# Kernel tuning notes

Measured on AMD Instinct MI355X. Metric: run time of the kernel, lower is better.

Reference implementation:

```python
import jax, jax.numpy as jnp
import numpy as np

TEXT_DIM = 768
IMAGE_DIM = 1024
HIDDEN = 2048
FF = 128
HEADS = 8
HEAD_DIM = HIDDEN // HEADS  # 256


def setup_inputs() -> dict:
    key = jax.random.key(0)
    ks = jax.random.split(key, 16)
    def lin(k, fan_in, fan_out):
        bound = 1.0 / np.sqrt(fan_in)
        kw, kb = jax.random.split(k)
        W = jax.random.uniform(kw, (fan_in, fan_out), jnp.float32, -bound, bound)
        b = jax.random.uniform(kb, (fan_out,), jnp.float32, -bound, bound)
        return W, b
    text = jax.random.normal(ks[0], (16, 512, TEXT_DIM), jnp.float32)
    image = jax.random.normal(ks[1], (16, 576, IMAGE_DIM), jnp.float32)
    wq, bq = lin(ks[2], TEXT_DIM, HIDDEN)
    wk, bk = lin(ks[3], IMAGE_DIM, HIDDEN)
    wv, bv = lin(ks[4], IMAGE_DIM, HIDDEN)
    wr, br = lin(ks[5], HIDDEN, TEXT_DIM)
    w1, b1 = lin(ks[6], TEXT_DIM, FF)
    w2, b2 = lin(ks[7], FF, TEXT_DIM)
    gamma = jnp.ones((TEXT_DIM,), jnp.float32)
    beta = jnp.zeros((TEXT_DIM,), jnp.float32)
    return {"text": text, "image": image,
            "wq": wq, "bq": bq, "wk": wk, "bk": bk, "wv": wv, "bv": bv,
            "wr": wr, "br": br, "w1": w1, "b1": b1, "w2": w2, "b2": b2,
            "gamma": gamma, "beta": beta}


def reference(text, image, wq, bq, wk, bk, wv, bv, wr, br, w1, b1, w2, b2, gamma, beta):
    # Dropout is identity (eval mode).
    bs, lt, _ = text.shape
    li = image.shape[1]
    Q = (text @ wq + bq).reshape(bs, lt, HEADS, HEAD_DIM)
    K = (image @ wk + bk).reshape(bs, li, HEADS, HEAD_DIM)
    V = (image @ wv + bv).reshape(bs, li, HEADS, HEAD_DIM)
    scale = jnp.sqrt(jnp.float32(HEAD_DIM))
    scores = jnp.einsum('bqhd,bkhd->bhqk', Q, K) / scale  # [B,H,Lt,Li]
    attn = jax.nn.softmax(scores, axis=-1)
    x = jnp.einsum('bhqk,bkhd->bqhd', attn, V).reshape(bs, lt, HIDDEN)
    out = x @ wr + br  # [B,Lt,text_dim]
    ff = jax.nn.relu(out @ w1 + b1) @ w2 + b2
    out = out + ff
    # LayerNorm over last dim (eps=1e-5, torch default)
    mu = jnp.mean(out, axis=-1, keepdims=True)
    var = jnp.mean(jnp.square(out - mu), axis=-1, keepdims=True)
    return (out - mu) / jnp.sqrt(var + 1e-5) * gamma + beta
```

## Files before the change

kernel.cpp:

```cpp
#include <hip/hip_runtime.h>
#include <stdint.h>
#include <stddef.h>

typedef __attribute__((ext_vector_type(8))) short bf16x8;
typedef __attribute__((ext_vector_type(4))) float f32x4;

typedef __attribute__((address_space(1))) unsigned int uint_g;
typedef __attribute__((address_space(3))) unsigned int uint_l;

#define DEV static __device__ __forceinline__

DEV unsigned short f2bf(float f) {
  unsigned int u = __float_as_uint(f);
  u += 0x7FFFu + ((u >> 16) & 1u);
  return (unsigned short)(u >> 16);
}

DEV void gl_lds16(const unsigned short* g, unsigned short* l) {
  __builtin_amdgcn_global_load_lds((const uint_g*)g, (uint_l*)l, 16, 0, 0);
}

__global__ __launch_bounds__(256) void k_f32_to_bf16(const float* __restrict__ in,
                                                     unsigned short* __restrict__ out, int n4) {
  int i = blockIdx.x * 256 + threadIdx.x;
  if (i >= n4) return;
  const float4 v = ((const float4*)in)[i];
  ushort4 o;
  o.x = f2bf(v.x); o.y = f2bf(v.y); o.z = f2bf(v.z); o.w = f2bf(v.w);
  ((ushort4*)out)[i] = o;
}

__global__ __launch_bounds__(256) void k_transpose_to_bf16(const float* __restrict__ in,
                                                           unsigned short* __restrict__ out,
                                                           int R, int C) {
  __shared__ unsigned short tile[32][33];
  const int c0 = blockIdx.x << 5, r0 = blockIdx.y << 5;
  const int tx = threadIdx.x & 31, ty = threadIdx.x >> 5;
  #pragma unroll
  for (int i = 0; i < 32; i += 8)
    tile[ty + i][tx] = f2bf(in[(size_t)(r0 + ty + i) * C + c0 + tx]);
  __syncthreads();
  #pragma unroll
  for (int i = 0; i < 32; i += 8)
    out[(size_t)(c0 + ty + i) * R + r0 + tx] = tile[tx][ty + i];
}

enum { EPI_BIAS = 0, EPI_VT = 3, EPI_DUAL = 4, EPI_RELU = 5, EPI_RES = 6 };

template <int BM, int BN, int EPI>
__global__ __launch_bounds__(256)
void k_gemm(const unsigned short* __restrict__ A, const unsigned short* __restrict__ B,
            int lda, int ldb, int kSteps,
            void* C0, void* C1, const float* bias, const float* resid, int ldc, float scale) {
  constexpr int TM = BM / 32;
  constexpr int TN = BN / 32;
  __shared__ unsigned short At[BM * 32];
  __shared__ unsigned short Bt[BN * 32];

  const int t = threadIdx.x;
  const int lane = t & 63, wave = t >> 6;
  const int wm = wave >> 1, wn = wave & 1;

  const unsigned short* Ab = A + (size_t)blockIdx.y * BM * lda;
  const unsigned short* Bb = B + (size_t)blockIdx.x * BN * ldb;

  const int frow = lane & 15, fk = (lane >> 4) << 3;

  f32x4 acc[TM][TN] = {};

  for (int ks = 0; ks < kSteps; ++ks) {
    const int k0 = ks << 5;
    __syncthreads();
    #pragma unroll
    for (int r = 0; r < BM / 64; ++r) {
      int off16 = (r << 8) + t;
      int row = off16 >> 2, kk = (off16 & 3) << 3;
      gl_lds16(Ab + (size_t)row * lda + k0 + kk, &At[(row << 5) + kk]);
    }
    #pragma unroll
    for (int r = 0; r < BN / 64; ++r) {
      int off16 = (r << 8) + t;
      int row = off16 >> 2, kk = (off16 & 3) << 3;
      gl_lds16(Bb + (size_t)row * ldb + k0 + kk, &Bt[(row << 5) + kk]);
    }
    __syncthreads();

    bf16x8 af[TM], bv[TN];
    #pragma unroll
    for (int mi = 0; mi < TM; ++mi)
      af[mi] = *(const bf16x8*)&At[((wm * (BM / 2) + mi * 16 + frow) << 5) + fk];
    #pragma unroll
    for (int ni = 0; ni < TN; ++ni)
      bv[ni] = *(const bf16x8*)&Bt[((wn * (BN / 2) + ni * 16 + frow) << 5) + fk];
    #pragma unroll
    for (int mi = 0; mi < TM; ++mi)
      #pragma unroll
      for (int ni = 0; ni < TN; ++ni)
        acc[mi][ni] = __builtin_amdgcn_mfma_f32_16x16x32_bf16(af[mi], bv[ni], acc[mi][ni], 0, 0, 0);
  }

  const int mb = blockIdx.y * BM + wm * (BM / 2) + ((lane >> 4) << 2);
  const int nb = blockIdx.x * BN + wn * (BN / 2) + (lane & 15);

  #pragma unroll
  for (int mi = 0; mi < TM; ++mi) {
    const int m = mb + mi * 16;
    #pragma unroll
    for (int ni = 0; ni < TN; ++ni) {
      const int n = nb + ni * 16;
      f32x4 v = acc[mi][ni];
      if constexpr (EPI == EPI_BIAS) {
        unsigned short* O = (unsigned short*)C0;
        const float bv2 = bias[n];
        #pragma unroll
        for (int r = 0; r < 4; ++r) O[(size_t)(m + r) * ldc + n] = f2bf((v[r] + bv2) * scale);
      } else if constexpr (EPI == EPI_VT) {
        const int b = m / 576, li = m - b * 576;
        const int h = n >> 8, d = n & 255;
        const float bv2 = bias[n];
        ushort4 o;
        o.x = f2bf(v[0] + bv2); o.y = f2bf(v[1] + bv2);
        o.z = f2bf(v[2] + bv2); o.w = f2bf(v[3] + bv2);
        *(ushort4*)((unsigned short*)C0 + ((size_t)((b * 8 + h) * 256 + d)) * 576 + li) = o;
      } else if constexpr (EPI == EPI_DUAL) {
        float* Of = (float*)C0;
        unsigned short* Ob = (unsigned short*)C1;
        const float bv2 = bias[n];
        #pragma unroll
        for (int r = 0; r < 4; ++r) {
          const float x = v[r] + bv2;
          const size_t idx = (size_t)(m + r) * ldc + n;
          Of[idx] = x; Ob[idx] = f2bf(x);
        }
      } else if constexpr (EPI == EPI_RELU) {
        unsigned short* O = (unsigned short*)C0;
        const float bv2 = bias[n];
        #pragma unroll
        for (int r = 0; r < 4; ++r) {
          const float x = v[r] + bv2;
          O[(size_t)(m + r) * ldc + n] = f2bf(x > 0.f ? x : 0.f);
        }
      } else if constexpr (EPI == EPI_RES) {
        float* Of = (float*)C0;
        const float bv2 = bias[n];
        #pragma unroll
        for (int r = 0; r < 4; ++r) {
          const size_t idx = (size_t)(m + r) * ldc + n;
          Of[idx] = v[r] + bv2 + resid[idx];
        }
      }
    }
  }
}

__global__ __launch_bounds__(512, 3)
void k_flash(const unsigned short* __restrict__ Q, const unsigned short* __restrict__ K,
             const unsigned short* __restrict__ Vt, unsigned short* __restrict__ X) {
  __shared__ unsigned short Ks[2][8 * 32 * 32];
  __shared__ unsigned short Vs[2][256 * 32];
  __shared__ unsigned short Ps[128 * 32];
  __shared__ unsigned short Ones[16 * 32];

  const int t = threadIdx.x, lane = t & 63, w = t >> 6;
  const int frow = lane & 15, quad = lane >> 4, fk = quad << 3;

  const int id = blockIdx.x;
  const int qb = (id >> 3) & 3;
  const int bh = (id & 7) | ((id >> 5) << 3);
  const int b = bh >> 3, h = bh & 7;
  const int q0 = qb << 7;

  const unsigned short* Kg = K + ((size_t)b * 576) * 2048 + h * 256;
  const unsigned short* Vg = Vt + (size_t)bh * 147456;

  Ones[t & 511] = ((t & 511) < 32) ? (unsigned short)0x3F80 : (unsigned short)0;

  const unsigned short* Qg =
      Q + ((size_t)(b * 512 + q0 + w * 16 + frow)) * 2048 + h * 256;
  bf16x8 Qf[8];
  #pragma unroll
  for (int kd = 0; kd < 8; ++kd)
    Qf[kd] = *(const bf16x8*)(Qg + kd * 32 + fk);

  f32x4 acc_o[17] = {};

  auto stage = [&](int s, int bufi) {
    const int li0 = s << 5;
    unsigned short* Kb = &Ks[bufi][0];
    unsigned short* Vb = &Vs[bufi][0];
    #pragma unroll
    for (int it = 0; it < 2; ++it) {
      int e = (it << 9) + t;
      int row = e >> 2, c = (e & 3) << 3;
      int kd = row >> 5, li = row & 31;
      gl_lds16(Kg + (size_t)(li0 + li) * 2048 + kd * 32 + c, &Kb[(row << 5) + c]);
    }
    #pragma unroll
    for (int it = 0; it < 2; ++it) {
      int e = (it << 9) + t;
      int d = e >> 2, c = (e & 3) << 3;
      gl_lds16(Vg + (size_t)d * 576 + li0 + c, &Vb[(d << 5) + c]);
    }
  };

  stage(0, 0);

  for (int s = 0; s < 18; ++s) {
    const int buf = s & 1;
    __syncthreads();
    if (s + 1 < 18) stage(s + 1, buf ^ 1);

    f32x4 acc_s[2] = {};
    #pragma unroll
    for (int kd = 0; kd < 8; ++kd) {
      #pragma unroll
      for (int ni = 0; ni < 2; ++ni) {
        const bf16x8 bv = *(const bf16x8*)&Ks[buf][((kd * 32 + ni * 16 + frow) << 5) + fk];
        acc_s[ni] = __builtin_amdgcn_mfma_f32_16x16x32_bf16(Qf[kd], bv, acc_s[ni], 0, 0, 0);
      }
    }

    #pragma unroll
    for (int ni = 0; ni < 2; ++ni)
      #pragma unroll
      for (int r = 0; r < 4; ++r)
        Ps[(((w << 4) + (quad << 2) + r) << 5) + ni * 16 + frow] = f2bf(__expf(acc_s[ni][r]));

    const bf16x8 af = *(const bf16x8*)&Ps[(((w << 4) + frow) << 5) + fk];
    #pragma unroll
    for (int ni = 0; ni < 16; ++ni) {
      const bf16x8 bv = *(const bf16x8*)&Vs[buf][((ni * 16 + frow) << 5) + fk];
      acc_o[ni] = __builtin_amdgcn_mfma_f32_16x16x32_bf16(af, bv, acc_o[ni], 0, 0, 0);
    }
    {
      const bf16x8 bv = *(const bf16x8*)&Ones[(frow << 5) + fk];
      acc_o[16] = __builtin_amdgcn_mfma_f32_16x16x32_bf16(af, bv, acc_o[16], 0, 0, 0);
    }
  }

  float linv[4];
  #pragma unroll
  for (int r = 0; r < 4; ++r)
    linv[r] = 1.0f / __shfl(acc_o[16][r], lane & 48);

  unsigned short* Xo = X + ((size_t)(b * 512 + q0 + (w << 4) + (quad << 2))) * 2048 +
                       h * 256 + frow;
  #pragma unroll
  for (int ni = 0; ni < 16; ++ni)
    #pragma unroll
    for (int r = 0; r < 4; ++r)
      Xo[(size_t)r * 2048 + ni * 16] = f2bf(acc_o[ni][r] * linv[r]);
}

__global__ __launch_bounds__(256) void k_layernorm768(float* O, const float* __restrict__ gamma,
                                                      const float* __restrict__ beta) {
  const int row = blockIdx.x;
  float* p = O + (size_t)row * 768;
  const int t = threadIdx.x;
  const int lane = t & 63, wave = t >> 6;
  const float x0 = p[t], x1 = p[t + 256], x2 = p[t + 512];
  float s = x0 + x1 + x2;
  float q = x0 * x0 + x1 * x1 + x2 * x2;
  #pragma unroll
  for (int i = 32; i >= 1; i >>= 1) { s += __shfl_xor(s, i); q += __shfl_xor(q, i); }
  __shared__ float rs[4], rq[4];
  if (lane == 0) { rs[wave] = s; rq[wave] = q; }
  __syncthreads();
  s = rs[0] + rs[1] + rs[2] + rs[3];
  q = rq[0] + rq[1] + rq[2] + rq[3];
  const float mu = s * (1.0f / 768.0f);
  const float var = q * (1.0f / 768.0f) - mu * mu;
  const float inv = rsqrtf(var + 1e-5f);
  p[t]       = (x0 - mu) * inv * gamma[t]       + beta[t];
  p[t + 256] = (x1 - mu) * inv * gamma[t + 256] + beta[t + 256];
  p[t + 512] = (x2 - mu) * inv * gamma[t + 512] + beta[t + 512];
}

extern "C" void kernel_launch(void* const* d_in, const int* in_sizes, int n_in,
                              void* d_out, int out_size, void* d_ws, size_t ws_size,
                              hipStream_t stream) {
  const float* text  = (const float*)d_in[0];
  const float* image = (const float*)d_in[1];
  const float* wq = (const float*)d_in[2];  const float* bq = (const float*)d_in[3];
  const float* wk = (const float*)d_in[4];  const float* bk = (const float*)d_in[5];
  const float* wv = (const float*)d_in[6];  const float* bv = (const float*)d_in[7];
  const float* wr = (const float*)d_in[8];  const float* br = (const float*)d_in[9];
  const float* w1 = (const float*)d_in[10]; const float* b1 = (const float*)d_in[11];
  const float* w2 = (const float*)d_in[12]; const float* b2 = (const float*)d_in[13];
  const float* gamma = (const float*)d_in[14]; const float* beta = (const float*)d_in[15];

  uint8_t* ws = (uint8_t*)d_ws;
  constexpr size_t o_Tbf = 0;
  constexpr size_t o_Ibf = 12582912;
  constexpr size_t o_X   = 0;
  constexpr size_t o_Q   = 33554432;
  constexpr size_t o_Kb  = o_Q   + 33554432;
  constexpr size_t o_Vt  = o_Kb  + 37748736;
  constexpr size_t o_wqT = o_Vt  + 37748736;
  constexpr size_t o_wkT = o_wqT + 3145728;
  constexpr size_t o_wvT = o_wkT + 4194304;
  constexpr size_t o_wrT = o_wvT + 4194304;
  constexpr size_t o_w1T = o_wrT + 3145728;
  constexpr size_t o_w2T = o_w1T + 196608;
  constexpr size_t o_OutB= o_w2T + 196608;
  constexpr size_t o_H   = o_OutB+ 12582912;

  unsigned short* Tbf  = (unsigned short*)(ws + o_Tbf);
  unsigned short* Ibf  = (unsigned short*)(ws + o_Ibf);
  unsigned short* Xb   = (unsigned short*)(ws + o_X);
  unsigned short* Qb   = (unsigned short*)(ws + o_Q);
  unsigned short* Kb   = (unsigned short*)(ws + o_Kb);
  unsigned short* Vt   = (unsigned short*)(ws + o_Vt);
  unsigned short* wqT  = (unsigned short*)(ws + o_wqT);
  unsigned short* wkT  = (unsigned short*)(ws + o_wkT);
  unsigned short* wvT  = (unsigned short*)(ws + o_wvT);
  unsigned short* wrT  = (unsigned short*)(ws + o_wrT);
  unsigned short* w1T  = (unsigned short*)(ws + o_w1T);
  unsigned short* w2T  = (unsigned short*)(ws + o_w2T);
  unsigned short* OutB = (unsigned short*)(ws + o_OutB);
  unsigned short* Hb   = (unsigned short*)(ws + o_H);
  float* OutF = (float*)d_out;

  const dim3 blk(256);

  k_f32_to_bf16<<<dim3(6144), blk, 0, stream>>>(text,  Tbf, 1572864);
  k_f32_to_bf16<<<dim3(9216), blk, 0, stream>>>(image, Ibf, 2359296);
  k_transpose_to_bf16<<<dim3(64, 24), blk, 0, stream>>>(wq, wqT, 768, 2048);
  k_transpose_to_bf16<<<dim3(64, 32), blk, 0, stream>>>(wk, wkT, 1024, 2048);
  k_transpose_to_bf16<<<dim3(64, 32), blk, 0, stream>>>(wv, wvT, 1024, 2048);
  k_transpose_to_bf16<<<dim3(24, 64), blk, 0, stream>>>(wr, wrT, 2048, 768);
  k_transpose_to_bf16<<<dim3(4, 24),  blk, 0, stream>>>(w1, w1T, 768, 128);
  k_transpose_to_bf16<<<dim3(24, 4),  blk, 0, stream>>>(w2, w2T, 128, 768);

  k_gemm<128, 128, EPI_BIAS><<<dim3(16, 64), blk, 0, stream>>>(
      Tbf, wqT, 768, 768, 24, Qb, nullptr, bq, nullptr, 2048, 0.0625f);
  k_gemm<128, 128, EPI_BIAS><<<dim3(16, 72), blk, 0, stream>>>(
      Ibf, wkT, 1024, 1024, 32, Kb, nullptr, bk, nullptr, 2048, 1.0f);
  k_gemm<128, 128, EPI_VT><<<dim3(16, 72), blk, 0, stream>>>(
      Ibf, wvT, 1024, 1024, 32, Vt, nullptr, bv, nullptr, 0, 1.0f);

  k_flash<<<dim3(512), dim3(512), 0, stream>>>(Qb, Kb, Vt, Xb);

  k_gemm<128, 128, EPI_DUAL><<<dim3(6, 64), blk, 0, stream>>>(
      Xb, wrT, 2048, 2048, 64, OutF, OutB, br, nullptr, 768, 1.0f);

  k_gemm<64, 64, EPI_RELU><<<dim3(2, 128), blk, 0, stream>>>(
      OutB, w1T, 768, 768, 24, Hb, nullptr, b1, nullptr, 128, 1.0f);

  k_gemm<128, 128, EPI_RES><<<dim3(6, 64), blk, 0, stream>>>(
      Hb, w2T, 128, 128, 4, OutF, nullptr, b2, (const float*)d_out, 768, 1.0f);

  k_layernorm768<<<dim3(8192), blk, 0, stream>>>(OutF, gamma, beta);

  (void)in_sizes; (void)n_in; (void)out_size; (void)ws_size;
}
```

Baseline: 520.1 us.

## Double-buffer GEMM LDS tiles and give each flash wave 32 query rows

The GEMM kernel now double-buffers its A/B LDS tiles so the next k-step's global-to-LDS loads run while the current step's MFMAs execute, dropping one barrier per step. The flash kernel now processes 256 query rows per block (32 per wave) with half the blocks, so each K/V tile loaded into LDS is reused across twice as many queries. The P tile is padded to a stride of 40 to reduce LDS bank conflicts. Softmax uses exp2 with log2(e) folded into the Q scale. The cost is higher register pressure (occupancy bound lowered to 2) and only 256 blocks for the flash kernel, plus doubled GEMM LDS use.

Measured after the change: 472.4 us. 9.2% less time.

```diff
diff --git a/kernel.cpp b/kernel.cpp
--- a/kernel.cpp
+++ b/kernel.cpp
@@ -54,8 +54,8 @@
             void* C0, void* C1, const float* bias, const float* resid, int ldc, float scale) {
   constexpr int TM = BM / 32;
   constexpr int TN = BN / 32;
-  __shared__ unsigned short At[BM * 32];
-  __shared__ unsigned short Bt[BN * 32];
+  __shared__ unsigned short At[2][BM * 32];
+  __shared__ unsigned short Bt[2][BN * 32];
 
   const int t = threadIdx.x;
   const int lane = t & 63, wave = t >> 6;
@@ -68,30 +68,36 @@
 
   f32x4 acc[TM][TN] = {};
 
-  for (int ks = 0; ks < kSteps; ++ks) {
+  auto stage = [&](int ks, int bi) {
     const int k0 = ks << 5;
-    __syncthreads();
     #pragma unroll
     for (int r = 0; r < BM / 64; ++r) {
       int off16 = (r << 8) + t;
       int row = off16 >> 2, kk = (off16 & 3) << 3;
-      gl_lds16(Ab + (size_t)row * lda + k0 + kk, &At[(row << 5) + kk]);
+      gl_lds16(Ab + (size_t)row * lda + k0 + kk, &At[bi][(row << 5) + kk]);
     }
     #pragma unroll
     for (int r = 0; r < BN / 64; ++r) {
       int off16 = (r << 8) + t;
       int row = off16 >> 2, kk = (off16 & 3) << 3;
-      gl_lds16(Bb + (size_t)row * ldb + k0 + kk, &Bt[(row << 5) + kk]);
-    }
+      gl_lds16(Bb + (size_t)row * ldb + k0 + kk, &Bt[bi][(row << 5) + kk]);
+    }
+  };
+
+  stage(0, 0);
+
+  for (int ks = 0; ks < kSteps; ++ks) {
+    const int buf = ks & 1;
     __syncthreads();
+    if (ks + 1 < kSteps) stage(ks + 1, buf ^ 1);
 
     bf16x8 af[TM], bv[TN];
     #pragma unroll
     for (int mi = 0; mi < TM; ++mi)
-      af[mi] = *(const bf16x8*)&At[((wm * (BM / 2) + mi * 16 + frow) << 5) + fk];
+      af[mi] = *(const bf16x8*)&At[buf][((wm * (BM / 2) + mi * 16 + frow) << 5) + fk];
     #pragma unroll
     for (int ni = 0; ni < TN; ++ni)
-      bv[ni] = *(const bf16x8*)&Bt[((wn * (BN / 2) + ni * 16 + frow) << 5) + fk];
+      bv[ni] = *(const bf16x8*)&Bt[buf][((wn * (BN / 2) + ni * 16 + frow) << 5) + fk];
     #pragma unroll
     for (int mi = 0; mi < TM; ++mi)
       #pragma unroll
@@ -153,41 +159,44 @@
   }
 }
 
-__global__ __launch_bounds__(512, 3)
+__global__ __launch_bounds__(512, 2)
 void k_flash(const unsigned short* __restrict__ Q, const unsigned short* __restrict__ K,
              const unsigned short* __restrict__ Vt, unsigned short* __restrict__ X) {
   __shared__ unsigned short Ks[2][8 * 32 * 32];
   __shared__ unsigned short Vs[2][256 * 32];
-  __shared__ unsigned short Ps[128 * 32];
-  __shared__ unsigned short Ones[16 * 32];
+  __shared__ unsigned short Ps[256 * 40];
+  __shared__ unsigned short Ones[512];
 
   const int t = threadIdx.x, lane = t & 63, w = t >> 6;
   const int frow = lane & 15, quad = lane >> 4, fk = quad << 3;
 
   const int id = blockIdx.x;
-  const int qb = (id >> 3) & 3;
-  const int bh = (id & 7) | ((id >> 5) << 3);
+  const int qb = (id >> 3) & 1;
+  const int bh = (id & 7) | ((id >> 4) << 3);
   const int b = bh >> 3, h = bh & 7;
-  const int q0 = qb << 7;
+  const int q0 = qb << 8;
 
   const unsigned short* Kg = K + ((size_t)b * 576) * 2048 + h * 256;
   const unsigned short* Vg = Vt + (size_t)bh * 147456;
 
-  Ones[t & 511] = ((t & 511) < 32) ? (unsigned short)0x3F80 : (unsigned short)0;
-
-  const unsigned short* Qg =
-      Q + ((size_t)(b * 512 + q0 + w * 16 + frow)) * 2048 + h * 256;
-  bf16x8 Qf[8];
-  #pragma unroll
-  for (int kd = 0; kd < 8; ++kd)
-    Qf[kd] = *(const bf16x8*)(Qg + kd * 32 + fk);
-
-  f32x4 acc_o[17] = {};
-
-  auto stage = [&](int s, int bufi) {
+  Ones[t] = (t < 32) ? (unsigned short)0x3F80 : (unsigned short)0;
+
+  bf16x8 Qf[2][8];
+  #pragma unroll
+  for (int half = 0; half < 2; ++half) {
+    const unsigned short* Qg =
+        Q + ((size_t)(b * 512 + q0 + w * 32 + half * 16 + frow)) * 2048 + h * 256;
+    #pragma unroll
+    for (int kd = 0; kd < 8; ++kd)
+      Qf[half][kd] = *(const bf16x8*)(Qg + kd * 32 + fk);
+  }
+
+  f32x4 acc_o[2][17] = {};
+
+  auto stage = [&](int s, int bi) {
     const int li0 = s << 5;
-    unsigned short* Kb = &Ks[bufi][0];
-    unsigned short* Vb = &Vs[bufi][0];
+    unsigned short* Kb = &Ks[bi][0];
+    unsigned short* Vb = &Vs[bi][0];
     #pragma unroll
     for (int it = 0; it < 2; ++it) {
       int e = (it << 9) + t;
@@ -205,51 +214,63 @@
 
   stage(0, 0);
 
+  const int prow = (w << 5) + (quad << 2);
+
   for (int s = 0; s < 18; ++s) {
     const int buf = s & 1;
     __syncthreads();
     if (s + 1 < 18) stage(s + 1, buf ^ 1);
 
-    f32x4 acc_s[2] = {};
+    f32x4 acc_s[2][2] = {};
     #pragma unroll
     for (int kd = 0; kd < 8; ++kd) {
       #pragma unroll
       for (int ni = 0; ni < 2; ++ni) {
         const bf16x8 bv = *(const bf16x8*)&Ks[buf][((kd * 32 + ni * 16 + frow) << 5) + fk];
-        acc_s[ni] = __builtin_amdgcn_mfma_f32_16x16x32_bf16(Qf[kd], bv, acc_s[ni], 0, 0, 0);
+        acc_s[0][ni] = __builtin_amdgcn_mfma_f32_16x16x32_bf16(Qf[0][kd], bv, acc_s[0][ni], 0, 0, 0);
+        acc_s[1][ni] = __builtin_amdgcn_mfma_f32_16x16x32_bf16(Qf[1][kd], bv, acc_s[1][ni], 0, 0, 0);
       }
     }
 
     #pragma unroll
-    for (int ni = 0; ni < 2; ++ni)
+    for (int half = 0; half < 2; ++half)
+      #pragma unroll
+      for (int ni = 0; ni < 2; ++ni)
+        #pragma unroll
+        for (int r = 0; r < 4; ++r)
+          Ps[(prow + half * 16 + r) * 40 + ni * 16 + frow] =
+              f2bf(__builtin_amdgcn_exp2f(acc_s[half][ni][r]));
+
+    bf16x8 paf[2];
+    paf[0] = *(const bf16x8*)&Ps[((w << 5) + frow) * 40 + fk];
+    paf[1] = *(const bf16x8*)&Ps[((w << 5) + 16 + frow) * 40 + fk];
+    #pragma unroll
+    for (int ni = 0; ni < 16; ++ni) {
+      const bf16x8 bv = *(const bf16x8*)&Vs[buf][((ni * 16 + frow) << 5) + fk];
+      acc_o[0][ni] = __builtin_amdgcn_mfma_f32_16x16x32_bf16(paf[0], bv, acc_o[0][ni], 0, 0, 0);
+      acc_o[1][ni] = __builtin_amdgcn_mfma_f32_16x16x32_bf16(paf[1], bv, acc_o[1][ni], 0, 0, 0);
+    }
+    {
+      const bf16x8 bv = *(const bf16x8*)&Ones[(frow << 5) + fk];
+      acc_o[0][16] = __builtin_amdgcn_mfma_f32_16x16x32_bf16(paf[0], bv, acc_o[0][16], 0, 0, 0);
+      acc_o[1][16] = __builtin_amdgcn_mfma_f32_16x16x32_bf16(paf[1], bv, acc_o[1][16], 0, 0, 0);
+    }
+  }
+
+  #pragma unroll
+  for (int half = 0; half < 2; ++half) {
+    float linv[4];
+    #pragma unroll
+    for (int r = 0; r < 4; ++r)
+      linv[r] = 1.0f / __shfl(acc_o[half][16][r], lane & 48);
+    unsigned short* Xo = X + ((size_t)(b * 512 + q0 + w * 32 + half * 16 + (quad << 2))) * 2048 +
+                         h * 256 + frow;
+    #pragma unroll
+    for (int ni = 0; ni < 16; ++ni)
       #pragma unroll
       for (int r = 0; r < 4; ++r)
-        Ps[(((w << 4) + (quad << 2) + r) << 5) + ni * 16 + frow] = f2bf(__expf(acc_s[ni][r]));
-
-    const bf16x8 af = *(const bf16x8*)&Ps[(((w << 4) + frow) << 5) + fk];
-    #pragma unroll
-    for (int ni = 0; ni < 16; ++ni) {
-      const bf16x8 bv = *(const bf16x8*)&Vs[buf][((ni * 16 + frow) << 5) + fk];
-      acc_o[ni] = __builtin_amdgcn_mfma_f32_16x16x32_bf16(af, bv, acc_o[ni], 0, 0, 0);
-    }
-    {
-      const bf16x8 bv = *(const bf16x8*)&Ones[(frow << 5) + fk];
-      acc_o[16] = __builtin_amdgcn_mfma_f32_16x16x32_bf16(af, bv, acc_o[16], 0, 0, 0);
-    }
-  }
-
-  float linv[4];
-  #pragma unroll
-  for (int r = 0; r < 4; ++r)
-    linv[r] = 1.0f / __shfl(acc_o[16][r], lane & 48);
-
-  unsigned short* Xo = X + ((size_t)(b * 512 + q0 + (w << 4) + (quad << 2))) * 2048 +
-                       h * 256 + frow;
-  #pragma unroll
-  for (int ni = 0; ni < 16; ++ni)
-    #pragma unroll
-    for (int r = 0; r < 4; ++r)
-      Xo[(size_t)r * 2048 + ni * 16] = f2bf(acc_o[ni][r] * linv[r]);
+        Xo[(size_t)r * 2048 + ni * 16] = f2bf(acc_o[half][ni][r] * linv[r]);
+  }
 }
 
 __global__ __launch_bounds__(256) void k_layernorm768(float* O, const float* __restrict__ gamma,
@@ -333,13 +354,13 @@
   k_transpose_to_bf16<<<dim3(24, 4),  blk, 0, stream>>>(w2, w2T, 128, 768);
 
   k_gemm<128, 128, EPI_BIAS><<<dim3(16, 64), blk, 0, stream>>>(
-      Tbf, wqT, 768, 768, 24, Qb, nullptr, bq, nullptr, 2048, 0.0625f);
+      Tbf, wqT, 768, 768, 24, Qb, nullptr, bq, nullptr, 2048, 0.0625f * 1.44269504f);
   k_gemm<128, 128, EPI_BIAS><<<dim3(16, 72), blk, 0, stream>>>(
       Ibf, wkT, 1024, 1024, 32, Kb, nullptr, bk, nullptr, 2048, 1.0f);
   k_gemm<128, 128, EPI_VT><<<dim3(16, 72), blk, 0, stream>>>(
       Ibf, wvT, 1024, 1024, 32, Vt, nullptr, bv, nullptr, 0, 1.0f);
 
-  k_flash<<<dim3(512), dim3(512), 0, stream>>>(Qb, Kb, Vt, Xb);
+  k_flash<<<dim3(256), dim3(512), 0, stream>>>(Qb, Kb, Vt, Xb);
 
   k_gemm<128, 128, EPI_DUAL><<<dim3(6, 64), blk, 0, stream>>>(
       Xb, wrT, 2048, 2048, 64, OutF, OutB, br, nullptr, 768, 1.0f);
```
